# Kernel optimization log

Hardware: AMD Instinct MI355X
Metric: run time of the kernel (lower is better)

Reference implementation:

```python
import jax, jax.numpy as jnp
import numpy as np

N, E, EL = 20000, 320000, 100000
IN, HID, OUT, H = 256, 128, 128, 4
NEG_SLOPE = 0.2


def setup_inputs() -> dict:
    key = jax.random.key(0)
    ks = jax.random.split(key, 20)
    g = lambda k, shape, fan: jax.random.normal(k, shape, jnp.float32) * (1.0 / np.sqrt(fan))
    inp = {
        'x': jax.random.normal(ks[0], (N, IN), jnp.float32),
        'edge_index': jax.random.randint(ks[1], (2, E), 0, N, jnp.int32),
        'edge_label_index': jax.random.randint(ks[2], (2, EL), 0, N, jnp.int32),
        # GATv2 layer 1: in -> hidden, heads=H, concat
        'W_l1': g(ks[3], (IN, H * HID), IN), 'b_l1': jnp.zeros((H * HID,), jnp.float32),
        'W_r1': g(ks[4], (IN, H * HID), IN), 'b_r1': jnp.zeros((H * HID,), jnp.float32),
        'att1': g(ks[5], (H, HID), HID), 'bias1': jnp.zeros((H * HID,), jnp.float32),
        # GATv2 layer 2: H*hidden -> out, heads=1
        'W_l2': g(ks[6], (H * HID, OUT), H * HID), 'b_l2': jnp.zeros((OUT,), jnp.float32),
        'W_r2': g(ks[7], (H * HID, OUT), H * HID), 'b_r2': jnp.zeros((OUT,), jnp.float32),
        'att2': g(ks[8], (1, OUT), OUT), 'bias2': jnp.zeros((OUT,), jnp.float32),
        # decoder: Linear(2*OUT, HID) -> GELU -> Linear(HID, 1)
        'W_d1': g(ks[9], (2 * OUT, HID), 2 * OUT), 'b_d1': jnp.zeros((HID,), jnp.float32),
        'W_d2': g(ks[10], (HID, 1), HID), 'b_d2': jnp.zeros((1,), jnp.float32),
    }
    return inp


def gatv2_conv(x, src, dst, Wl, bl, Wr, br, att, bias, heads, ch):
    n = x.shape[0]
    xl = (x @ Wl + bl).reshape(n, heads, ch)  # source transform
    xr = (x @ Wr + br).reshape(n, heads, ch)  # target transform
    xj = xl[src]                              # [E, H, C] messages from source
    xi = xr[dst]                              # [E, H, C]
    e = jax.nn.leaky_relu(xi + xj, NEG_SLOPE)
    logits = jnp.einsum('ehc,hc->eh', e, att)  # [E, H]
    # segment softmax over incoming edges of each target node
    m = jax.ops.segment_max(logits, dst, num_segments=n)
    a = jnp.exp(logits - m[dst])
    s = jax.ops.segment_sum(a, dst, num_segments=n)
    alpha = a / s[dst]
    out = jax.ops.segment_sum(alpha[..., None] * xj, dst, num_segments=n)
    return out.reshape(n, heads * ch) + bias


def reference(x, edge_index, edge_label_index,
              W_l1, b_l1, W_r1, b_r1, att1, bias1,
              W_l2, b_l2, W_r2, b_r2, att2, bias2,
              W_d1, b_d1, W_d2, b_d2):
    n = x.shape[0]
    loops = jnp.arange(n, dtype=edge_index.dtype)
    src = jnp.concatenate([edge_index[0], loops])  # add_self_loops=True (PyG default)
    dst = jnp.concatenate([edge_index[1], loops])
    z = gatv2_conv(x, src, dst, W_l1, b_l1, W_r1, b_r1, att1, bias1, H, HID)
    z = jax.nn.gelu(z)  # dropout is identity in eval mode
    z = gatv2_conv(z, src, dst, W_l2, b_l2, W_r2, b_r2, att2, bias2, 1, OUT)
    # link decoder: gather-concat-MLP
    h = jnp.concatenate([z[edge_label_index[0]], z[edge_label_index[1]]], axis=-1)
    h = jax.nn.gelu(h @ W_d1 + b_d1)
    return (h @ W_d2 + b_d2).squeeze(-1)
```

## Files before the change

### kernel.cpp

```cpp
#include <hip/hip_runtime.h>
#include <hip/hip_bf16.h>
#include <math.h>
#include <stdint.h>

using bf16 = __hip_bfloat16;
typedef unsigned short u16;
typedef unsigned int   u32;
typedef __attribute__((ext_vector_type(8))) short short8;
typedef __attribute__((ext_vector_type(4))) float f32x4;
typedef _Float16 h2 __attribute__((ext_vector_type(2)));

static constexpr int NN   = 20000;
static constexpr int EE   = 320000;
static constexpr int ELN  = 100000;
static constexpr int ETOT = EE + NN;
static constexpr int INC  = 256;
static constexpr int C1   = 512;
static constexpr int C2   = 128;
static constexpr int NB   = (NN + 255) / 256;

__device__ __forceinline__ float us2f(u16 u){ union{u32 i; float f;}x; x.i=((u32)u)<<16; return x.f; }
__device__ __forceinline__ u16  f2us(float f){ union{bf16 h; u16 u;}c; c.h=__float2bfloat16(f); return c.u; }
__device__ __forceinline__ float h2f(u16 u){ union{u16 u; _Float16 h;}c; c.u=u; return (float)c.h; }
__device__ __forceinline__ float gelu_f(float x){
  float u = 1.5957691216057308f*(x + 0.044715f*x*x*x);
  float ex = __expf(u);
  float th = 1.f - 2.f/(ex + 1.f);
  return 0.5f*x*(1.f+th);
}
__device__ __forceinline__ void gl_lds16(const u16* g, void* l) {
  __builtin_amdgcn_global_load_lds((const __attribute__((address_space(1))) void*)g,
                                   (__attribute__((address_space(3))) void*)l, 16, 0, 0);
}
__device__ __forceinline__ void ld4v(const float* p, float* o){ float4 v=*(const float4*)p; o[0]=v.x;o[1]=v.y;o[2]=v.z;o[3]=v.w; }
__device__ __forceinline__ void ld4v(const u16* p, float* o){ uint2 v=*(const uint2*)p;
  o[0]=us2f(v.x&0xffff);o[1]=us2f(v.x>>16);o[2]=us2f(v.y&0xffff);o[3]=us2f(v.y>>16); }
__device__ __forceinline__ void ld4v(const _Float16* p, float* o){ uint2 v=*(const uint2*)p;
  o[0]=h2f(v.x&0xffff);o[1]=h2f(v.x>>16);o[2]=h2f(v.y&0xffff);o[3]=h2f(v.y>>16); }
__device__ __forceinline__ void ld8v(const float* p, float* o){ ld4v(p,o); ld4v(p+4,o+4); }
__device__ __forceinline__ void ld8v(const u16* p, float* o){ uint4 v=*(const uint4*)p;
  o[0]=us2f(v.x&0xffff);o[1]=us2f(v.x>>16);o[2]=us2f(v.y&0xffff);o[3]=us2f(v.y>>16);
  o[4]=us2f(v.z&0xffff);o[5]=us2f(v.z>>16);o[6]=us2f(v.w&0xffff);o[7]=us2f(v.w>>16); }
__device__ __forceinline__ void ld8v(const _Float16* p, float* o){ uint4 v=*(const uint4*)p;
  o[0]=h2f(v.x&0xffff);o[1]=h2f(v.x>>16);o[2]=h2f(v.y&0xffff);o[3]=h2f(v.y>>16);
  o[4]=h2f(v.z&0xffff);o[5]=h2f(v.z>>16);o[6]=h2f(v.w&0xffff);o[7]=h2f(v.w>>16); }
__device__ __forceinline__ void ld2v(const float* p, float* o){ float2 v=*(const float2*)p; o[0]=v.x;o[1]=v.y; }
__device__ __forceinline__ void ld2v(const _Float16* p, float* o){ u32 w=*(const u32*)p;
  o[0]=h2f(w&0xffff); o[1]=h2f(w>>16); }
__device__ __forceinline__ void st4v(float* p, const float* v){ *(float4*)p = make_float4(v[0],v[1],v[2],v[3]); }
__device__ __forceinline__ void st4v(u16* p, const float* v){ uint2 o;
  o.x=f2us(v[0])|((u32)f2us(v[1])<<16); o.y=f2us(v[2])|((u32)f2us(v[3])<<16); *(uint2*)p=o; }
__device__ __forceinline__ void st8v(float* p, const float* v){ st4v(p,v); st4v(p+4,v+4); }
__device__ __forceinline__ void st8v(u16* p, const float* v){ uint4 o;
  o.x=f2us(v[0])|((u32)f2us(v[1])<<16); o.y=f2us(v[2])|((u32)f2us(v[3])<<16);
  o.z=f2us(v[4])|((u32)f2us(v[5])<<16); o.w=f2us(v[6])|((u32)f2us(v[7])<<16); *(uint4*)p=o; }

struct PrepArgs {
  const float* x; u16* xth; u16* xtl; int nx;
  const float* wsrc[6]; u16* wth[6]; u16* wtl[6]; int wK[6]; int wN[6];
  const int* ei; int* cnt;
};
__global__ __launch_bounds__(256) void k_prep(PrepArgs a) {
  int seg = blockIdx.y;
  int tid = blockIdx.x*256 + threadIdx.x;
  int stride = gridDim.x*256;
  if (seg == 0) {
    for (int i = tid; i < a.nx; i += stride) {
      float v = a.x[i];
      u16 h = f2us(v);
      a.xth[i] = h;
      a.xtl[i] = f2us(v - us2f(h));
    }
  } else if (seg <= 6) {
    int s = seg - 1;
    int K = a.wK[s], N = a.wN[s];
    int n = K * N;
    for (int i = tid; i < n; i += stride) {
      int nn = i / K, k = i - nn*K;
      float v = a.wsrc[s][(size_t)k*N + nn];
      u16 h = f2us(v);
      a.wth[s][i] = h;
      a.wtl[s][i] = f2us(v - us2f(h));
    }
  } else {
    for (int e = tid; e < ETOT; e += stride) {
      int d = (e < EE) ? a.ei[EE + e] : (e - EE);
      if ((u32)d < (u32)NN) atomicAdd(&a.cnt[d], 1);
    }
  }
}

__global__ void k_scan_a(const int* __restrict__ cnt, int* __restrict__ row_ptr,
                         int* __restrict__ bsum) {
  __shared__ int buf[256];
  int idx = blockIdx.x*256 + threadIdx.x;
  int v = (idx < NN) ? cnt[idx] : 0;
  buf[threadIdx.x] = v;
  __syncthreads();
  for (int off = 1; off < 256; off <<= 1) {
    int t = (threadIdx.x >= off) ? buf[threadIdx.x - off] : 0;
    __syncthreads();
    buf[threadIdx.x] += t;
    __syncthreads();
  }
  if (idx < NN) row_ptr[idx] = buf[threadIdx.x] - v;
  if (threadIdx.x == 255) bsum[blockIdx.x] = buf[255];
}
__global__ void k_scan_b(int* __restrict__ bsum, int* __restrict__ row_ptr) {
  __shared__ int buf[128];
  int v = (threadIdx.x < NB) ? bsum[threadIdx.x] : 0;
  buf[threadIdx.x] = v;
  __syncthreads();
  for (int off = 1; off < 128; off <<= 1) {
    int t = (threadIdx.x >= off) ? buf[threadIdx.x - off] : 0;
    __syncthreads();
    buf[threadIdx.x] += t;
    __syncthreads();
  }
  if (threadIdx.x < NB) bsum[threadIdx.x] = buf[threadIdx.x] - v;
  if (threadIdx.x == 127) row_ptr[NN] = buf[127];
}
__global__ void k_scan_c(int* __restrict__ row_ptr, const int* __restrict__ bsum,
                         int* __restrict__ cur) {
  int idx = blockIdx.x*256 + threadIdx.x;
  if (idx < NN) {
    int v = row_ptr[idx] + bsum[blockIdx.x];
    row_ptr[idx] = v;
    cur[idx] = v;
  }
}
__global__ void k_scatter(const int* __restrict__ ei, int* __restrict__ cur,
                          int* __restrict__ col) {
  int e = blockIdx.x*blockDim.x + threadIdx.x;
  if (e < ETOT) {
    int s, d;
    if (e < EE) { s = ei[e]; d = ei[EE + e]; } else { s = d = e - EE; }
    if ((u32)d >= (u32)NN) d = 0;
    int pos = atomicAdd(&cur[d], 1);
    if ((u32)pos < (u32)ETOT) col[pos] = s;
  }
}

__global__ __launch_bounds__(256, 3)
void k_mgemm_a(const u16* __restrict__ Ath, const u16* __restrict__ Atl,
               const u16* __restrict__ Bth, const u16* __restrict__ Btl,
               const float* __restrict__ biasA, const float* __restrict__ biasB, int ncut,
               _Float16* __restrict__ C, int M, int N, int K, int nby) {
  __shared__ __align__(16) u16 sm[17408];
  int tid = threadIdx.x;
  int bidy = blockIdx.x % nby, bidx = blockIdx.x / nby;
  int m0 = bidx * 128, n0 = bidy * 128;
  int wave = tid >> 6, lane = tid & 63;
  int wm = (wave & 1) * 64, wn = (wave >> 1) * 64;
  int l15 = lane & 15, quad = lane >> 4;
  const u16* pbase = (wave == 0) ? Ath : (wave == 1) ? Atl : (wave == 2) ? Bth : Btl;
  bool isA = wave < 2;
  int rbase = isA ? m0 : n0;
  int rseg = lane >> 2;
  int kseg = (lane & 3) * 8;
  f32x4 acc[4][4] = {};
  for (int k0 = 0; k0 < K; k0 += 32) {
    #pragma unroll
    for (int i = 0; i < 8; ++i) {
      int r = rbase + i*16 + rseg;
      if (isA && r > M-1) r = M-1;
      gl_lds16(&pbase[(size_t)r*K + k0 + kseg], (char*)sm + (wave<<13) + (i<<10));
    }
    __syncthreads();
    short8 af_h[4], af_l[4], bf_h[4], bf_l[4];
    #pragma unroll
    for (int i = 0; i < 4; ++i) {
      af_h[i] = *(const short8*)&sm[         (wm + i*16 + l15)*32 + quad*8];
      af_l[i] = *(const short8*)&sm[ 4096 +  (wm + i*16 + l15)*32 + quad*8];
      bf_h[i] = *(const short8*)&sm[ 8192 +  (wn + i*16 + l15)*32 + quad*8];
      bf_l[i] = *(const short8*)&sm[12288 +  (wn + i*16 + l15)*32 + quad*8];
    }
    #pragma unroll
    for (int i = 0; i < 4; ++i)
      #pragma unroll
      for (int j = 0; j < 4; ++j) {
        acc[i][j] = __builtin_amdgcn_mfma_f32_16x16x32_bf16(af_h[i], bf_l[j], acc[i][j], 0,0,0);
        acc[i][j] = __builtin_amdgcn_mfma_f32_16x16x32_bf16(af_l[i], bf_h[j], acc[i][j], 0,0,0);
        acc[i][j] = __builtin_amdgcn_mfma_f32_16x16x32_bf16(af_h[i], bf_h[j], acc[i][j], 0,0,0);
      }
    __syncthreads();
  }
  #pragma unroll
  for (int j = 0; j < 4; ++j) {
    int col = wn + j*16 + l15;
    int colg = n0 + col;
    float bv = (colg < ncut) ? biasA[colg] : (biasB ? biasB[colg - ncut] : 0.f);
    #pragma unroll
    for (int i = 0; i < 4; ++i) {
      int rowb = wm + i*16 + quad*4;
      #pragma unroll
      for (int r = 0; r < 4; ++r) {
        union { _Float16 h; u16 u; } cv;
        cv.h = (_Float16)(acc[i][j][r] + bv);
        sm[(rowb + r)*136 + col] = cv.u;
      }
    }
  }
  __syncthreads();
  int row = tid >> 1, half = (tid & 1) * 64;
  int gr = m0 + row;
  if (gr < M) {
    uint4* d = (uint4*)&C[(size_t)gr*N + n0 + half];
    const uint4* s = (const uint4*)&sm[row*136 + half];
    #pragma unroll
    for (int q = 0; q < 8; ++q) d[q] = s[q];
  }
}

__global__ __launch_bounds__(256) void k_dec5(const _Float16* __restrict__ UV,
                                              const int* __restrict__ eli,
                                              const float* __restrict__ Wd2,
                                              const float* __restrict__ bd2,
                                              float* __restrict__ out) {
  int gw = (blockIdx.x*256 + threadIdx.x) >> 6;
  int nw = (gridDim.x*256) >> 6;
  int lane = threadIdx.x & 63;
  int c2 = lane*2;
  float w2a = Wd2[c2], w2b = Wd2[c2+1];
  float b2 = bd2[0];
  for (int e = gw; e < ELN; e += nw) {
    int a = __builtin_amdgcn_readfirstlane(eli[e]);      if ((u32)a >= (u32)NN) a = 0;
    int b = __builtin_amdgcn_readfirstlane(eli[ELN+e]);  if ((u32)b >= (u32)NN) b = 0;
    float u[2], v[2];
    ld2v(&UV[(size_t)a*256 + c2], u);
    ld2v(&UV[(size_t)b*256 + 128 + c2], v);
    float p = gelu_f(u[0]+v[0])*w2a + gelu_f(u[1]+v[1])*w2b;
    p += __shfl_xor(p,1);  p += __shfl_xor(p,2);
    p += __shfl_xor(p,4);  p += __shfl_xor(p,8);
    p += __shfl_xor(p,16); p += __shfl_xor(p,32);
    if (lane == 0) out[e] = p + b2;
  }
}

__global__ __launch_bounds__(256) void k_edge1p(const _Float16* __restrict__ xl,
                                                const _Float16* __restrict__ xr, int ld,
                                                const float* __restrict__ att,
                                                const float* __restrict__ bias,
                                                const int* __restrict__ row_ptr,
                                                const int* __restrict__ col,
                                                u16* __restrict__ z1h, u16* __restrict__ z1l) {
  int wid = (blockIdx.x*blockDim.x + threadIdx.x) >> 6;
  if (wid >= NN) return;
  int lane = threadIdx.x & 63;
  int c8 = lane*8;
  union Q { uint4 u; h2 h[4]; };
  Q XI; XI.u = *(const uint4*)&xr[(size_t)wid*ld + c8];
  h2 at[4];
  #pragma unroll
  for (int k=0;k<4;++k) { at[k][0] = (_Float16)att[c8+2*k]; at[k][1] = (_Float16)att[c8+2*k+1]; }
  const h2 k02 = {(_Float16)0.2f, (_Float16)0.2f};
  float acc[8] = {};
  float s = 0.f;
  int e0 = __builtin_amdgcn_readfirstlane(row_ptr[wid]);
  int e1 = __builtin_amdgcn_readfirstlane(row_ptr[wid+1]);
  int e = e0;
  for (; e + 4 <= e1; e += 4) {
    int s1 = __builtin_amdgcn_readfirstlane(col[e]);   if ((u32)s1 >= (u32)NN) s1 = 0;
    int s2 = __builtin_amdgcn_readfirstlane(col[e+1]); if ((u32)s2 >= (u32)NN) s2 = 0;
    int s3 = __builtin_amdgcn_readfirstlane(col[e+2]); if ((u32)s3 >= (u32)NN) s3 = 0;
    int s4 = __builtin_amdgcn_readfirstlane(col[e+3]); if ((u32)s4 >= (u32)NN) s4 = 0;
    Q X1, X2, X3, X4;
    X1.u = *(const uint4*)&xl[(size_t)s1*ld + c8];
    X2.u = *(const uint4*)&xl[(size_t)s2*ld + c8];
    X3.u = *(const uint4*)&xl[(size_t)s3*ld + c8];
    X4.u = *(const uint4*)&xl[(size_t)s4*ld + c8];
    float p1 = 0.f, p2 = 0.f, p3 = 0.f, p4 = 0.f;
    #pragma unroll
    for (int k=0;k<4;++k) {
      h2 t1 = XI.h[k] + X1.h[k]; t1 = __builtin_elementwise_max(t1, t1*k02);
      p1 = __builtin_amdgcn_fdot2(t1, at[k], p1, false);
      h2 t2 = XI.h[k] + X2.h[k]; t2 = __builtin_elementwise_max(t2, t2*k02);
      p2 = __builtin_amdgcn_fdot2(t2, at[k], p2, false);
      h2 t3 = XI.h[k] + X3.h[k]; t3 = __builtin_elementwise_max(t3, t3*k02);
      p3 = __builtin_amdgcn_fdot2(t3, at[k], p3, false);
      h2 t4 = XI.h[k] + X4.h[k]; t4 = __builtin_elementwise_max(t4, t4*k02);
      p4 = __builtin_amdgcn_fdot2(t4, at[k], p4, false);
    }
    p1 += __shfl_xor(p1,1); p2 += __shfl_xor(p2,1); p3 += __shfl_xor(p3,1); p4 += __shfl_xor(p4,1);
    p1 += __shfl_xor(p1,2); p2 += __shfl_xor(p2,2); p3 += __shfl_xor(p3,2); p4 += __shfl_xor(p4,2);
    p1 += __shfl_xor(p1,4); p2 += __shfl_xor(p2,4); p3 += __shfl_xor(p3,4); p4 += __shfl_xor(p4,4);
    p1 += __shfl_xor(p1,8); p2 += __shfl_xor(p2,8); p3 += __shfl_xor(p3,8); p4 += __shfl_xor(p4,8);
    float w1 = __expf(p1), w2 = __expf(p2), w3 = __expf(p3), w4 = __expf(p4);
    s += (w1 + w2) + (w3 + w4);
    #pragma unroll
    for (int k=0;k<4;++k) {
      acc[2*k]   += (w1*(float)X1.h[k][0] + w2*(float)X2.h[k][0])
                  + (w3*(float)X3.h[k][0] + w4*(float)X4.h[k][0]);
      acc[2*k+1] += (w1*(float)X1.h[k][1] + w2*(float)X2.h[k][1])
                  + (w3*(float)X3.h[k][1] + w4*(float)X4.h[k][1]);
    }
  }
  for (; e < e1; ++e) {
    int sn = __builtin_amdgcn_readfirstlane(col[e]); if ((u32)sn >= (u32)NN) sn = 0;
    Q XJ; XJ.u = *(const uint4*)&xl[(size_t)sn*ld + c8];
    float p = 0.f;
    #pragma unroll
    for (int k=0;k<4;++k) {
      h2 t = XI.h[k] + XJ.h[k];
      t = __builtin_elementwise_max(t, t*k02);
      p = __builtin_amdgcn_fdot2(t, at[k], p, false);
    }
    p += __shfl_xor(p,1); p += __shfl_xor(p,2);
    p += __shfl_xor(p,4); p += __shfl_xor(p,8);
    float w = __expf(p);
    s += w;
    #pragma unroll
    for (int k=0;k<4;++k) {
      acc[2*k]   += w*(float)XJ.h[k][0];
      acc[2*k+1] += w*(float)XJ.h[k][1];
    }
  }
  float inv = 1.f/s;
  u16 hh[8], ll[8];
  #pragma unroll
  for (int j=0;j<8;++j) {
    float o = gelu_f(acc[j]*inv + bias[c8+j]);
    hh[j] = f2us(o);
    ll[j] = f2us(o - us2f(hh[j]));
  }
  uint4 H, L;
  H.x = hh[0]|((u32)hh[1]<<16); H.y = hh[2]|((u32)hh[3]<<16);
  H.z = hh[4]|((u32)hh[5]<<16); H.w = hh[6]|((u32)hh[7]<<16);
  L.x = ll[0]|((u32)ll[1]<<16); L.y = ll[2]|((u32)ll[3]<<16);
  L.z = ll[4]|((u32)ll[5]<<16); L.w = ll[6]|((u32)ll[7]<<16);
  *(uint4*)&z1h[(size_t)wid*C1 + c8] = H;
  *(uint4*)&z1l[(size_t)wid*C1 + c8] = L;
}

__global__ __launch_bounds__(256) void k_edge2p(const _Float16* __restrict__ xl,
                                                const _Float16* __restrict__ xr, int ld,
                                                const float* __restrict__ att,
                                                const float* __restrict__ bias,
                                                const int* __restrict__ row_ptr,
                                                const int* __restrict__ col,
                                                u16* __restrict__ z2h, u16* __restrict__ z2l) {
  int wid = (blockIdx.x*blockDim.x + threadIdx.x) >> 6;
  if (wid >= NN) return;
  int lane = threadIdx.x & 63;
  int c2 = lane*2;
  union W { u32 u; h2 h; };
  W XI; XI.u = *(const u32*)&xr[(size_t)wid*ld + c2];
  h2 at; at[0] = (_Float16)att[c2]; at[1] = (_Float16)att[c2+1];
  const h2 k02 = {(_Float16)0.2f, (_Float16)0.2f};
  float s = 0.f, ac0 = 0.f, ac1 = 0.f;
  int e0 = __builtin_amdgcn_readfirstlane(row_ptr[wid]);
  int e1 = __builtin_amdgcn_readfirstlane(row_ptr[wid+1]);
  int e = e0;
  for (; e + 4 <= e1; e += 4) {
    int s1 = __builtin_amdgcn_readfirstlane(col[e]);   if ((u32)s1 >= (u32)NN) s1 = 0;
    int s2 = __builtin_amdgcn_readfirstlane(col[e+1]); if ((u32)s2 >= (u32)NN) s2 = 0;
    int s3 = __builtin_amdgcn_readfirstlane(col[e+2]); if ((u32)s3 >= (u32)NN) s3 = 0;
    int s4 = __builtin_amdgcn_readfirstlane(col[e+3]); if ((u32)s4 >= (u32)NN) s4 = 0;
    W X1, X2, X3, X4;
    X1.u = *(const u32*)&xl[(size_t)s1*ld + c2];
    X2.u = *(const u32*)&xl[(size_t)s2*ld + c2];
    X3.u = *(const u32*)&xl[(size_t)s3*ld + c2];
    X4.u = *(const u32*)&xl[(size_t)s4*ld + c2];
    h2 t1 = XI.h + X1.h; t1 = __builtin_elementwise_max(t1, t1*k02);
    h2 t2 = XI.h + X2.h; t2 = __builtin_elementwise_max(t2, t2*k02);
    h2 t3 = XI.h + X3.h; t3 = __builtin_elementwise_max(t3, t3*k02);
    h2 t4 = XI.h + X4.h; t4 = __builtin_elementwise_max(t4, t4*k02);
    float p1 = __builtin_amdgcn_fdot2(t1, at, 0.f, false);
    float p2 = __builtin_amdgcn_fdot2(t2, at, 0.f, false);
    float p3 = __builtin_amdgcn_fdot2(t3, at, 0.f, false);
    float p4 = __builtin_amdgcn_fdot2(t4, at, 0.f, false);
    p1 += __shfl_xor(p1,1);  p2 += __shfl_xor(p2,1);  p3 += __shfl_xor(p3,1);  p4 += __shfl_xor(p4,1);
    p1 += __shfl_xor(p1,2);  p2 += __shfl_xor(p2,2);  p3 += __shfl_xor(p3,2);  p4 += __shfl_xor(p4,2);
    p1 += __shfl_xor(p1,4);  p2 += __shfl_xor(p2,4);  p3 += __shfl_xor(p3,4);  p4 += __shfl_xor(p4,4);
    p1 += __shfl_xor(p1,8);  p2 += __shfl_xor(p2,8);  p3 += __shfl_xor(p3,8);  p4 += __shfl_xor(p4,8);
    p1 += __shfl_xor(p1,16); p2 += __shfl_xor(p2,16); p3 += __shfl_xor(p3,16); p4 += __shfl_xor(p4,16);
    p1 += __shfl_xor(p1,32); p2 += __shfl_xor(p2,32); p3 += __shfl_xor(p3,32); p4 += __shfl_xor(p4,32);
    float w1 = __expf(p1), w2 = __expf(p2), w3 = __expf(p3), w4 = __expf(p4);
    s += (w1 + w2) + (w3 + w4);
    ac0 += (w1*(float)X1.h[0] + w2*(float)X2.h[0]) + (w3*(float)X3.h[0] + w4*(float)X4.h[0]);
    ac1 += (w1*(float)X1.h[1] + w2*(float)X2.h[1]) + (w3*(float)X3.h[1] + w4*(float)X4.h[1]);
  }
  for (; e < e1; ++e) {
    int sn = __builtin_amdgcn_readfirstlane(col[e]); if ((u32)sn >= (u32)NN) sn = 0;
    W XJ; XJ.u = *(const u32*)&xl[(size_t)sn*ld + c2];
    h2 t = XI.h + XJ.h;
    t = __builtin_elementwise_max(t, t*k02);
    float p = __builtin_amdgcn_fdot2(t, at, 0.f, false);
    p += __shfl_xor(p,1);  p += __shfl_xor(p,2);
    p += __shfl_xor(p,4);  p += __shfl_xor(p,8);
    p += __shfl_xor(p,16); p += __shfl_xor(p,32);
    float w = __expf(p);
    s += w;
    ac0 += w*(float)XJ.h[0];
    ac1 += w*(float)XJ.h[1];
  }
  float inv = 1.f/s;
  float o0 = ac0*inv + bias[c2];
  float o1 = ac1*inv + bias[c2+1];
  u16 h0 = f2us(o0), h1 = f2us(o1);
  u16 l0 = f2us(o0 - us2f(h0)), l1v = f2us(o1 - us2f(h1));
  *(u32*)&z2h[(size_t)wid*C2 + c2] = h0 | ((u32)h1 << 16);
  *(u32*)&z2l[(size_t)wid*C2 + c2] = l0 | ((u32)l1v << 16);
}

__global__ void k_hist(const int* __restrict__ ei, int* __restrict__ cnt) {
  int e = blockIdx.x*blockDim.x + threadIdx.x;
  if (e < ETOT) {
    int d = (e < EE) ? ei[EE + e] : (e - EE);
    if ((u32)d < (u32)NN) atomicAdd(&cnt[d], 1);
  }
}
template <typename AT, typename CT>
__global__ __launch_bounds__(256) void k_gemm(const AT* __restrict__ A,
                                              const float* __restrict__ W,
                                              const float* __restrict__ bias,
                                              CT* __restrict__ C,
                                              int M, int Nc, int K) {
  __shared__ __align__(16) float As[16][64];
  __shared__ __align__(16) float Bs[16][64];
  int tid = threadIdx.x;
  int m0 = blockIdx.x*64, n0 = blockIdx.y*64;
  int ty = tid >> 4, tx = tid & 15;
  int lrow = tid >> 2;
  int lk   = (tid & 3)*4;
  int wk   = tid >> 4;
  int wn   = (tid & 15)*4;
  float acc[4][4] = {};
  for (int k0 = 0; k0 < K; k0 += 16) {
    int row = m0 + lrow;
    if (row < M) {
      float a4[4]; ld4v(&A[(size_t)row*K + k0 + lk], a4);
      As[lk+0][lrow]=a4[0]; As[lk+1][lrow]=a4[1]; As[lk+2][lrow]=a4[2]; As[lk+3][lrow]=a4[3];
    } else {
      #pragma unroll
      for (int j=0;j<4;++j) As[lk+j][lrow]=0.f;
    }
    {
      float4 bv4 = *(const float4*)&W[(size_t)(k0+wk)*Nc + n0 + wn];
      Bs[wk][wn+0]=bv4.x; Bs[wk][wn+1]=bv4.y; Bs[wk][wn+2]=bv4.z; Bs[wk][wn+3]=bv4.w;
    }
    __syncthreads();
    #pragma unroll
    for (int kk=0;kk<16;++kk) {
      float4 av = *(const float4*)&As[kk][ty*4];
      float4 bv = *(const float4*)&Bs[kk][tx*4];
      float a[4]={av.x,av.y,av.z,av.w}, b[4]={bv.x,bv.y,bv.z,bv.w};
      #pragma unroll
      for (int i=0;i<4;++i)
        #pragma unroll
        for (int j=0;j<4;++j)
          acc[i][j] += a[i]*b[j];
    }
    __syncthreads();
  }
  float bv[4];
  #pragma unroll
  for (int j=0;j<4;++j) bv[j] = bias[n0 + tx*4 + j];
  #pragma unroll
  for (int i=0;i<4;++i) {
    int row = m0 + ty*4 + i;
    if (row < M) {
      float o4[4] = {acc[i][0]+bv[0], acc[i][1]+bv[1], acc[i][2]+bv[2], acc[i][3]+bv[3]};
      st4v(&C[(size_t)row*Nc + n0 + tx*4], o4);
    }
  }
}
template <typename TI, typename TO>
__global__ __launch_bounds__(256) void k_edge1c(const TI* __restrict__ xl,
                                                const TI* __restrict__ xr, int ld,
                                                const float* __restrict__ att,
                                                const float* __restrict__ bias,
                                                const int* __restrict__ row_ptr,
                                                const int* __restrict__ col,
                                                TO* __restrict__ z1) {
  int wid = (blockIdx.x*blockDim.x + threadIdx.x) >> 6;
  if (wid >= NN) return;
  int lane = threadIdx.x & 63;
  int c8 = lane*8;
  float xi[8], av[8], acc[8] = {};
  ld8v(&xr[(size_t)wid*ld + c8], xi);
  #pragma unroll
  for (int j=0;j<8;++j) av[j] = att[c8+j];
  float s = 0.f;
  int e0 = row_ptr[wid], e1 = row_ptr[wid+1];
  for (int e = e0; e < e1; ++e) {
    int sn = col[e]; if ((u32)sn >= (u32)NN) sn = 0;
    float xj[8];
    ld8v(&xl[(size_t)sn*ld + c8], xj);
    float p = 0.f;
    #pragma unroll
    for (int j=0;j<8;++j) {
      float t = xi[j] + xj[j];
      t = fmaxf(t, 0.2f*t);
      p += t*av[j];
    }
    p += __shfl_xor(p,1); p += __shfl_xor(p,2);
    p += __shfl_xor(p,4); p += __shfl_xor(p,8);
    float w = __expf(p);
    s += w;
    #pragma unroll
    for (int j=0;j<8;++j) acc[j] += w*xj[j];
  }
  float inv = 1.f/s, o[8];
  #pragma unroll
  for (int j=0;j<8;++j) o[j] = gelu_f(acc[j]*inv + bias[c8+j]);
  st8v(&z1[(size_t)wid*C1 + c8], o);
}
template <typename TI, typename TO>
__global__ __launch_bounds__(256) void k_edge2c(const TI* __restrict__ xl,
                                                const TI* __restrict__ xr, int ld,
                                                const float* __restrict__ att,
                                                const float* __restrict__ bias,
                                                const int* __restrict__ row_ptr,
                                                const int* __restrict__ col,
                                                TO* __restrict__ z2) {
  int wid = (blockIdx.x*blockDim.x + threadIdx.x) >> 6;
  if (wid >= NN) return;
  int lane = threadIdx.x & 63;
  int c2 = lane*2;
  float xiv[2];
  ld2v(&xr[(size_t)wid*ld + c2], xiv);
  float a0 = att[c2], a1 = att[c2+1];
  float s = 0.f, ac0 = 0.f, ac1 = 0.f;
  int e0 = row_ptr[wid], e1 = row_ptr[wid+1];
  for (int e = e0; e < e1; ++e) {
    int sn = col[e]; if ((u32)sn >= (u32)NN) sn = 0;
    float xj[2];
    ld2v(&xl[(size_t)sn*ld + c2], xj);
    float t0 = xiv[0] + xj[0]; t0 = fmaxf(t0, 0.2f*t0);
    float t1 = xiv[1] + xj[1]; t1 = fmaxf(t1, 0.2f*t1);
    float p = t0*a0 + t1*a1;
    p += __shfl_xor(p,1);  p += __shfl_xor(p,2);
    p += __shfl_xor(p,4);  p += __shfl_xor(p,8);
    p += __shfl_xor(p,16); p += __shfl_xor(p,32);
    float w = __expf(p);
    s += w;
    ac0 += w*xj[0];
    ac1 += w*xj[1];
  }
  float inv = 1.f/s;
  z2[(size_t)wid*C2 + c2]   = (TO)(ac0*inv + bias[c2]);
  z2[(size_t)wid*C2 + c2+1] = (TO)(ac1*inv + bias[c2+1]);
}
__global__ __launch_bounds__(256) void k_dec2(const float* __restrict__ z2,
                                              const int* __restrict__ eli,
                                              const float* __restrict__ Wd1,
                                              const float* __restrict__ bd1,
                                              const float* __restrict__ Wd2,
                                              const float* __restrict__ bd2,
                                              float* __restrict__ out) {
  __shared__ __align__(16) float As[16][64];
  __shared__ __align__(16) float Bs[16][128];
  int tid = threadIdx.x;
  int e0 = blockIdx.x * 64;
  int ty = tid >> 4, tx = tid & 15;
  int lrow = tid >> 2;
  int lk   = (tid & 3) * 4;
  int wk   = tid >> 4;
  int wn   = (tid & 15) * 8;
  int e = e0 + lrow;
  bool ev = e < ELN;
  int ia = ev ? eli[e] : 0;       if ((u32)ia >= (u32)NN) ia = 0;
  int ib = ev ? eli[ELN+e] : 0;   if ((u32)ib >= (u32)NN) ib = 0;
  float acc[4][8] = {};
  for (int k0 = 0; k0 < 256; k0 += 16) {
    int kk4 = k0 + lk;
    const float* src = (kk4 < 128) ? &z2[(size_t)ia*128 + kk4]
                                   : &z2[(size_t)ib*128 + (kk4 - 128)];
    float4 a4 = ev ? *(const float4*)src : make_float4(0.f,0.f,0.f,0.f);
    As[lk+0][lrow]=a4.x; As[lk+1][lrow]=a4.y; As[lk+2][lrow]=a4.z; As[lk+3][lrow]=a4.w;
    *(float4*)&Bs[wk][wn]   = *(const float4*)&Wd1[(size_t)(k0+wk)*128 + wn];
    *(float4*)&Bs[wk][wn+4] = *(const float4*)&Wd1[(size_t)(k0+wk)*128 + wn + 4];
    __syncthreads();
    #pragma unroll
    for (int kk = 0; kk < 16; ++kk) {
      float4 av = *(const float4*)&As[kk][ty*4];
      float a[4] = {av.x, av.y, av.z, av.w};
      float4 b0 = *(const float4*)&Bs[kk][tx*4];
      float4 b1 = *(const float4*)&Bs[kk][64 + tx*4];
      float b[8] = {b0.x,b0.y,b0.z,b0.w,b1.x,b1.y,b1.z,b1.w};
      #pragma unroll
      for (int i = 0; i < 4; ++i)
        #pragma unroll
        for (int j = 0; j < 8; ++j)
          acc[i][j] += a[i]*b[j];
    }
    __syncthreads();
  }
  float w2[8], bb[8];
  #pragma unroll
  for (int j = 0; j < 4; ++j) {
    w2[j]   = Wd2[tx*4+j];      bb[j]   = bd1[tx*4+j];
    w2[j+4] = Wd2[64+tx*4+j];   bb[j+4] = bd1[64+tx*4+j];
  }
  float b2 = bd2[0];
  #pragma unroll
  for (int i = 0; i < 4; ++i) {
    float part = 0.f;
    #pragma unroll
    for (int j = 0; j < 8; ++j)
      part += gelu_f(acc[i][j] + bb[j]) * w2[j];
    part += __shfl_xor(part,1); part += __shfl_xor(part,2);
    part += __shfl_xor(part,4); part += __shfl_xor(part,8);
    int row = e0 + ty*4 + i;
    if (tx == 0 && row < ELN) out[row] = part + b2;
  }
}

__global__ void k_tiny(float* out, float code) {
  if (threadIdx.x == 0) out[0] = code;
}

extern "C" void kernel_launch(void* const* d_in, const int* in_sizes, int n_in,
                              void* d_out, int out_size, void* d_ws, size_t ws_size,
                              hipStream_t stream) {
  const float* x     = (const float*)d_in[0];
  const int*   ei    = (const int*)  d_in[1];
  const int*   eli   = (const int*)  d_in[2];
  const float* Wl1   = (const float*)d_in[3];
  const float* bl1   = (const float*)d_in[4];
  const float* Wr1   = (const float*)d_in[5];
  const float* br1   = (const float*)d_in[6];
  const float* att1  = (const float*)d_in[7];
  const float* bias1 = (const float*)d_in[8];
  const float* Wl2   = (const float*)d_in[9];
  const float* bl2   = (const float*)d_in[10];
  const float* Wr2   = (const float*)d_in[11];
  const float* br2   = (const float*)d_in[12];
  const float* att2  = (const float*)d_in[13];
  const float* bias2 = (const float*)d_in[14];
  const float* Wd1   = (const float*)d_in[15];
  const float* bd1   = (const float*)d_in[16];
  const float* Wd2   = (const float*)d_in[17];
  const float* bd2   = (const float*)d_in[18];
  float* out = (float*)d_out;

  constexpr size_t INTW = (size_t)(NN+1) + NN + ETOT;
  constexpr size_t FULL_WORDS = 3ull*NN*C1 + INTW;
  constexpr size_t CMP_WORDS  = 3ull*NN*C1/2 + INTW;

  bool full    = ws_size >= FULL_WORDS*4;
  bool compact = !full && ws_size >= CMP_WORDS*4;
  if (!full && !compact) {
    size_t mb = ws_size >> 20;
    k_tiny<<<1, 64, 0, stream>>>(out, 16384.f + (float)mb);
    return;
  }

  size_t regA = full ? (size_t)NN*C1 : (size_t)NN*C1/2;
  char* base = (char*)d_ws;
  void* wA = base;
  void* wB = base + regA*4;
  void* wC = base + 2*regA*4;
  int* row_ptr = (int*)(base + 3*regA*4);
  int* cnt     = row_ptr + (NN + 1);
  int* col     = cnt + NN;
  int* bsum    = (int*)wA;

  hipMemsetAsync(cnt, 0, NN*sizeof(int), stream);

  if (full) {
    _Float16* xlr1 = (_Float16*)wA;
    _Float16* xlr2 = (_Float16*)wA;
    _Float16* UV   = (_Float16*)wA;
    u16* xth = (u16*)wB;
    u16* xtl = xth + (size_t)NN*INC;
    u16* wt1th = (u16*)((char*)wB + (21u<<20));
    u16* wt1tl = wt1th + 1024*256;
    u16* wt2th = wt1tl + 1024*256;
    u16* wt2tl = wt2th + 256*512;
    u16* wdth  = wt2tl + 256*512;
    u16* wdtl  = wdth  + 256*128;
    u16* z1h = (u16*)wC;
    u16* z1l = z1h + (size_t)NN*C1;
    u16* z2h = (u16*)wC;
    u16* z2l = z2h + (size_t)NN*C2;

    PrepArgs pa;
    pa.x = x; pa.xth = xth; pa.xtl = xtl; pa.nx = NN*INC;
    pa.wsrc[0]=Wl1;          pa.wth[0]=wt1th;         pa.wtl[0]=wt1tl;         pa.wK[0]=INC; pa.wN[0]=C1;
    pa.wsrc[1]=Wr1;          pa.wth[1]=wt1th+512*256; pa.wtl[1]=wt1tl+512*256; pa.wK[1]=INC; pa.wN[1]=C1;
    pa.wsrc[2]=Wl2;          pa.wth[2]=wt2th;         pa.wtl[2]=wt2tl;         pa.wK[2]=C1;  pa.wN[2]=C2;
    pa.wsrc[3]=Wr2;          pa.wth[3]=wt2th+128*512; pa.wtl[3]=wt2tl+128*512; pa.wK[3]=C1;  pa.wN[3]=C2;
    pa.wsrc[4]=Wd1;          pa.wth[4]=wdth;          pa.wtl[4]=wdtl;          pa.wK[4]=128; pa.wN[4]=128;
    pa.wsrc[5]=Wd1+128*128;  pa.wth[5]=wdth+128*128;  pa.wtl[5]=wdtl+128*128;  pa.wK[5]=128; pa.wN[5]=128;
    pa.ei = ei; pa.cnt = cnt;
    k_prep<<<dim3(1344, 8), 256, 0, stream>>>(pa);

    k_scan_a<<<NB, 256, 0, stream>>>(cnt, row_ptr, bsum);
    k_scan_b<<<1, 128, 0, stream>>>(bsum, row_ptr);
    k_scan_c<<<NB, 256, 0, stream>>>(row_ptr, bsum, cnt);
    k_scatter<<<(ETOT+255)/256, 256, 0, stream>>>(ei, cnt, col);

    k_mgemm_a<<<157*8, 256, 0, stream>>>(xth, xtl, wt1th, wt1tl,
                                         bl1, br1, 512, xlr1, NN, 1024, INC, 8);
    k_edge1p<<<NN/4, 256, 0, stream>>>(xlr1, xlr1+512, 1024, att1, bias1, row_ptr, col, z1h, z1l);
    k_mgemm_a<<<157*2, 256, 0, stream>>>(z1h, z1l, wt2th, wt2tl,
                                         bl2, br2, 128, xlr2, NN, 256, C1, 2);
    k_edge2p<<<NN/4, 256, 0, stream>>>(xlr2, xlr2+128, 256, att2, bias2, row_ptr, col, z2h, z2l);
    k_mgemm_a<<<157*2, 256, 0, stream>>>(z2h, z2l, wdth, wdtl,
                                         bd1, nullptr, 128, UV, NN, 256, 128, 2);
    k_dec5<<<2048, 256, 0, stream>>>(UV, eli, Wd2, bd2, out);
  } else {
    u16* xl1 = (u16*)wA;
    u16* xr1 = (u16*)wB;
    u16* z1  = (u16*)wC;
    float* xl2 = (float*)wA;
    float* xr2 = (float*)wB;
    float* z2  = (float*)wC;
    k_hist<<<(ETOT+255)/256, 256, 0, stream>>>(ei, cnt);
    k_scan_a<<<NB, 256, 0, stream>>>(cnt, row_ptr, bsum);
    k_scan_b<<<1, 128, 0, stream>>>(bsum, row_ptr);
    k_scan_c<<<NB, 256, 0, stream>>>(row_ptr, bsum, cnt);
    k_scatter<<<(ETOT+255)/256, 256, 0, stream>>>(ei, cnt, col);
    dim3 g1((NN+63)/64, C1/64);
    dim3 g2((NN+63)/64, C2/64);
    k_gemm<float,u16><<<g1, 256, 0, stream>>>(x, Wl1, bl1, xl1, NN, C1, INC);
    k_gemm<float,u16><<<g1, 256, 0, stream>>>(x, Wr1, br1, xr1, NN, C1, INC);
    k_edge1c<u16,u16><<<NN/4, 256, 0, stream>>>(xl1, xr1, C1, att1, bias1, row_ptr, col, z1);
    k_gemm<u16,float><<<g2, 256, 0, stream>>>(z1, Wl2, bl2, xl2, NN, C2, C1);
    k_gemm<u16,float><<<g2, 256, 0, stream>>>(z1, Wr2, br2, xr2, NN, C2, C1);
    k_edge2c<float,float><<<NN/4, 256, 0, stream>>>(xl2, xr2, C2, att2, bias2, row_ptr, col, z2);
    k_dec2<<<(ELN+63)/64, 256, 0, stream>>>(z2, eli, Wd1, bd1, Wd2, bd2, out);
  }
}
```

Before: 347.8 us.

## Split layer-1 edge aggregation of each node across four waves with LDS reduction

The layer-1 GATv2 edge kernel now assigns one 256-thread block per target node instead of one wave per node. The node's incoming edges are split into four contiguous chunks, one per wave, and the partial weighted sums and softmax denominators are combined through shared memory before wave 0 applies GELU and writes the output. This aims to shorten the serial gather chain per node and expose more memory parallelism. In exchange it adds a block barrier, shared-memory traffic and four times as many blocks, and waves sit idle when a node has very few edges. The softmax still skips max-subtraction, as before.

After: 348.4 us. No clear change (+0.2%).

```diff
diff --git a/kernel.cpp b/kernel.cpp
--- a/kernel.cpp
+++ b/kernel.cpp
@@ -237,16 +237,17 @@
   }
 }
 
-__global__ __launch_bounds__(256) void k_edge1p(const _Float16* __restrict__ xl,
+__global__ __launch_bounds__(256) void k_edge1s(const _Float16* __restrict__ xl,
                                                 const _Float16* __restrict__ xr, int ld,
                                                 const float* __restrict__ att,
                                                 const float* __restrict__ bias,
                                                 const int* __restrict__ row_ptr,
                                                 const int* __restrict__ col,
                                                 u16* __restrict__ z1h, u16* __restrict__ z1l) {
-  int wid = (blockIdx.x*blockDim.x + threadIdx.x) >> 6;
-  if (wid >= NN) return;
-  int lane = threadIdx.x & 63;
+  __shared__ float pacc[3][8][64];
+  __shared__ float psum[3][64];
+  int wid = blockIdx.x;
+  int wave = threadIdx.x >> 6, lane = threadIdx.x & 63;
   int c8 = lane*8;
   union Q { uint4 u; h2 h[4]; };
   Q XI; XI.u = *(const uint4*)&xr[(size_t)wid*ld + c8];
@@ -258,8 +259,11 @@
   float s = 0.f;
   int e0 = __builtin_amdgcn_readfirstlane(row_ptr[wid]);
   int e1 = __builtin_amdgcn_readfirstlane(row_ptr[wid+1]);
-  int e = e0;
-  for (; e + 4 <= e1; e += 4) {
+  int q = ((e1 - e0) + 3) >> 2;
+  int st = e0 + wave*q;
+  int en = st + q; if (en > e1) en = e1; if (st > e1) st = e1;
+  int e = st;
+  for (; e + 4 <= en; e += 4) {
     int s1 = __builtin_amdgcn_readfirstlane(col[e]);   if ((u32)s1 >= (u32)NN) s1 = 0;
     int s2 = __builtin_amdgcn_readfirstlane(col[e+1]); if ((u32)s2 >= (u32)NN) s2 = 0;
     int s3 = __builtin_amdgcn_readfirstlane(col[e+2]); if ((u32)s3 >= (u32)NN) s3 = 0;
@@ -295,7 +299,7 @@
                   + (w3*(float)X3.h[k][1] + w4*(float)X4.h[k][1]);
     }
   }
-  for (; e < e1; ++e) {
+  for (; e < en; ++e) {
     int sn = __builtin_amdgcn_readfirstlane(col[e]); if ((u32)sn >= (u32)NN) sn = 0;
     Q XJ; XJ.u = *(const uint4*)&xl[(size_t)sn*ld + c8];
     float p = 0.f;
@@ -315,21 +319,35 @@
       acc[2*k+1] += w*(float)XJ.h[k][1];
     }
   }
-  float inv = 1.f/s;
-  u16 hh[8], ll[8];
-  #pragma unroll
-  for (int j=0;j<8;++j) {
-    float o = gelu_f(acc[j]*inv + bias[c8+j]);
-    hh[j] = f2us(o);
-    ll[j] = f2us(o - us2f(hh[j]));
-  }
-  uint4 H, L;
-  H.x = hh[0]|((u32)hh[1]<<16); H.y = hh[2]|((u32)hh[3]<<16);
-  H.z = hh[4]|((u32)hh[5]<<16); H.w = hh[6]|((u32)hh[7]<<16);
-  L.x = ll[0]|((u32)ll[1]<<16); L.y = ll[2]|((u32)ll[3]<<16);
-  L.z = ll[4]|((u32)ll[5]<<16); L.w = ll[6]|((u32)ll[7]<<16);
-  *(uint4*)&z1h[(size_t)wid*C1 + c8] = H;
-  *(uint4*)&z1l[(size_t)wid*C1 + c8] = L;
+  if (wave > 0) {
+    #pragma unroll
+    for (int j=0;j<8;++j) pacc[wave-1][j][lane] = acc[j];
+    psum[wave-1][lane] = s;
+  }
+  __syncthreads();
+  if (wave == 0) {
+    #pragma unroll
+    for (int wv=0; wv<3; ++wv) {
+      s += psum[wv][lane];
+      #pragma unroll
+      for (int j=0;j<8;++j) acc[j] += pacc[wv][j][lane];
+    }
+    float inv = 1.f/s;
+    u16 hh[8], ll[8];
+    #pragma unroll
+    for (int j=0;j<8;++j) {
+      float o = gelu_f(acc[j]*inv + bias[c8+j]);
+      hh[j] = f2us(o);
+      ll[j] = f2us(o - us2f(hh[j]));
+    }
+    uint4 H, L;
+    H.x = hh[0]|((u32)hh[1]<<16); H.y = hh[2]|((u32)hh[3]<<16);
+    H.z = hh[4]|((u32)hh[5]<<16); H.w = hh[6]|((u32)hh[7]<<16);
+    L.x = ll[0]|((u32)ll[1]<<16); L.y = ll[2]|((u32)ll[3]<<16);
+    L.z = ll[4]|((u32)ll[5]<<16); L.w = ll[6]|((u32)ll[7]<<16);
+    *(uint4*)&z1h[(size_t)wid*C1 + c8] = H;
+    *(uint4*)&z1l[(size_t)wid*C1 + c8] = L;
+  }
 }
 
 __global__ __launch_bounds__(256) void k_edge2p(const _Float16* __restrict__ xl,
@@ -694,7 +712,7 @@
 
     k_mgemm_a<<<157*8, 256, 0, stream>>>(xth, xtl, wt1th, wt1tl,
                                          bl1, br1, 512, xlr1, NN, 1024, INC, 8);
-    k_edge1p<<<NN/4, 256, 0, stream>>>(xlr1, xlr1+512, 1024, att1, bias1, row_ptr, col, z1h, z1l);
+    k_edge1s<<<NN, 256, 0, stream>>>(xlr1, xlr1+512, 1024, att1, bias1, row_ptr, col, z1h, z1l);
     k_mgemm_a<<<157*2, 256, 0, stream>>>(z1h, z1l, wt2th, wt2tl,
                                          bl2, br2, 128, xlr2, NN, 256, C1, 2);
     k_edge2p<<<NN/4, 256, 0, stream>>>(xlr2, xlr2+128, 256, att2, bias2, row_ptr, col, z2h, z2l);
```

## Replace LDS-staged 128x128 split-bf16 GEMM with single-wave direct-load 64x64 tiles

Applied to the files above, without the earlier changes.

The three split-precision GEMMs move from a 256-thread block that stages 128x128 A/B tiles in shared memory through global_load_lds, with barriers, to a one-wave block that loads MFMA fragments straight from global memory into registers for a 64x64 tile. This removes the LDS staging and per-k-step barriers and launches many more small blocks, but drops cross-wave reuse of the staged tiles, so each operand is read from global/L2 more often. Separately, the layer-1 edge aggregation loop goes from 4-way to 2-way unrolled, with a single-edge prologue for odd degrees, which trades memory-level parallelism for lower register pressure.

Result: slower. 414.4 us (+19.2%).

```diff
diff --git a/kernel.cpp b/kernel.cpp
--- a/kernel.cpp
+++ b/kernel.cpp
@@ -27,10 +27,6 @@
   float ex = __expf(u);
   float th = 1.f - 2.f/(ex + 1.f);
   return 0.5f*x*(1.f+th);
-}
-__device__ __forceinline__ void gl_lds16(const u16* g, void* l) {
-  __builtin_amdgcn_global_load_lds((const __attribute__((address_space(1))) void*)g,
-                                   (__attribute__((address_space(3))) void*)l, 16, 0, 0);
 }
 __device__ __forceinline__ void ld4v(const float* p, float* o){ float4 v=*(const float4*)p; o[0]=v.x;o[1]=v.y;o[2]=v.z;o[3]=v.w; }
 __device__ __forceinline__ void ld4v(const u16* p, float* o){ uint2 v=*(const uint2*)p;
@@ -141,74 +137,60 @@
   }
 }
 
-__global__ __launch_bounds__(256, 3)
-void k_mgemm_a(const u16* __restrict__ Ath, const u16* __restrict__ Atl,
+__global__ __launch_bounds__(64)
+void k_mgemm_d(const u16* __restrict__ Ath, const u16* __restrict__ Atl,
                const u16* __restrict__ Bth, const u16* __restrict__ Btl,
                const float* __restrict__ biasA, const float* __restrict__ biasB, int ncut,
-               _Float16* __restrict__ C, int M, int N, int K, int nby) {
-  __shared__ __align__(16) u16 sm[17408];
-  int tid = threadIdx.x;
-  int bidy = blockIdx.x % nby, bidx = blockIdx.x / nby;
-  int m0 = bidx * 128, n0 = bidy * 128;
-  int wave = tid >> 6, lane = tid & 63;
-  int wm = (wave & 1) * 64, wn = (wave >> 1) * 64;
+               _Float16* __restrict__ C, int M, int N, int K, int nt) {
+  __shared__ __align__(16) u16 tile[64*72];
+  int lane = threadIdx.x;
   int l15 = lane & 15, quad = lane >> 4;
-  const u16* pbase = (wave == 0) ? Ath : (wave == 1) ? Atl : (wave == 2) ? Bth : Btl;
-  bool isA = wave < 2;
-  int rbase = isA ? m0 : n0;
-  int rseg = lane >> 2;
-  int kseg = (lane & 3) * 8;
+  int m0 = (blockIdx.x / nt) * 64;
+  int n0 = (blockIdx.x % nt) * 64;
   f32x4 acc[4][4] = {};
   for (int k0 = 0; k0 < K; k0 += 32) {
-    #pragma unroll
-    for (int i = 0; i < 8; ++i) {
-      int r = rbase + i*16 + rseg;
-      if (isA && r > M-1) r = M-1;
-      gl_lds16(&pbase[(size_t)r*K + k0 + kseg], (char*)sm + (wave<<13) + (i<<10));
-    }
-    __syncthreads();
-    short8 af_h[4], af_l[4], bf_h[4], bf_l[4];
+    short8 ah[4], al[4], bh[4], bl[4];
     #pragma unroll
     for (int i = 0; i < 4; ++i) {
-      af_h[i] = *(const short8*)&sm[         (wm + i*16 + l15)*32 + quad*8];
-      af_l[i] = *(const short8*)&sm[ 4096 +  (wm + i*16 + l15)*32 + quad*8];
-      bf_h[i] = *(const short8*)&sm[ 8192 +  (wn + i*16 + l15)*32 + quad*8];
-      bf_l[i] = *(const short8*)&sm[12288 +  (wn + i*16 + l15)*32 + quad*8];
+      int ra = m0 + i*16 + l15; if (ra > M-1) ra = M-1;
+      int rb = n0 + i*16 + l15;
+      size_t oa = (size_t)ra*K + k0 + quad*8;
+      size_t ob = (size_t)rb*K + k0 + quad*8;
+      ah[i] = *(const short8*)&Ath[oa];
+      al[i] = *(const short8*)&Atl[oa];
+      bh[i] = *(const short8*)&Bth[ob];
+      bl[i] = *(const short8*)&Btl[ob];
     }
     #pragma unroll
     for (int i = 0; i < 4; ++i)
       #pragma unroll
       for (int j = 0; j < 4; ++j) {
-        acc[i][j] = __builtin_amdgcn_mfma_f32_16x16x32_bf16(af_h[i], bf_l[j], acc[i][j], 0,0,0);
-        acc[i][j] = __builtin_amdgcn_mfma_f32_16x16x32_bf16(af_l[i], bf_h[j], acc[i][j], 0,0,0);
-        acc[i][j] = __builtin_amdgcn_mfma_f32_16x16x32_bf16(af_h[i], bf_h[j], acc[i][j], 0,0,0);
+        acc[i][j] = __builtin_amdgcn_mfma_f32_16x16x32_bf16(ah[i], bl[j], acc[i][j], 0,0,0);
+        acc[i][j] = __builtin_amdgcn_mfma_f32_16x16x32_bf16(al[i], bh[j], acc[i][j], 0,0,0);
+        acc[i][j] = __builtin_amdgcn_mfma_f32_16x16x32_bf16(ah[i], bh[j], acc[i][j], 0,0,0);
       }
-    __syncthreads();
   }
   #pragma unroll
   for (int j = 0; j < 4; ++j) {
-    int col = wn + j*16 + l15;
-    int colg = n0 + col;
+    int colg = n0 + j*16 + l15;
     float bv = (colg < ncut) ? biasA[colg] : (biasB ? biasB[colg - ncut] : 0.f);
     #pragma unroll
     for (int i = 0; i < 4; ++i) {
-      int rowb = wm + i*16 + quad*4;
       #pragma unroll
       for (int r = 0; r < 4; ++r) {
         union { _Float16 h; u16 u; } cv;
         cv.h = (_Float16)(acc[i][j][r] + bv);
-        sm[(rowb + r)*136 + col] = cv.u;
+        tile[(i*16 + quad*4 + r)*72 + j*16 + l15] = cv.u;
       }
     }
   }
   __syncthreads();
-  int row = tid >> 1, half = (tid & 1) * 64;
-  int gr = m0 + row;
-  if (gr < M) {
-    uint4* d = (uint4*)&C[(size_t)gr*N + n0 + half];
-    const uint4* s = (const uint4*)&sm[row*136 + half];
-    #pragma unroll
-    for (int q = 0; q < 8; ++q) d[q] = s[q];
+  int row = m0 + lane;
+  if (row < M) {
+    uint4* d = (uint4*)&C[(size_t)row*N + n0];
+    const u16* s = &tile[lane*72];
+    #pragma unroll
+    for (int q = 0; q < 8; ++q) d[q] = *(const uint4*)(s + q*8);
   }
 }
 
@@ -259,43 +241,7 @@
   int e0 = __builtin_amdgcn_readfirstlane(row_ptr[wid]);
   int e1 = __builtin_amdgcn_readfirstlane(row_ptr[wid+1]);
   int e = e0;
-  for (; e + 4 <= e1; e += 4) {
-    int s1 = __builtin_amdgcn_readfirstlane(col[e]);   if ((u32)s1 >= (u32)NN) s1 = 0;
-    int s2 = __builtin_amdgcn_readfirstlane(col[e+1]); if ((u32)s2 >= (u32)NN) s2 = 0;
-    int s3 = __builtin_amdgcn_readfirstlane(col[e+2]); if ((u32)s3 >= (u32)NN) s3 = 0;
-    int s4 = __builtin_amdgcn_readfirstlane(col[e+3]); if ((u32)s4 >= (u32)NN) s4 = 0;
-    Q X1, X2, X3, X4;
-    X1.u = *(const uint4*)&xl[(size_t)s1*ld + c8];
-    X2.u = *(const uint4*)&xl[(size_t)s2*ld + c8];
-    X3.u = *(const uint4*)&xl[(size_t)s3*ld + c8];
-    X4.u = *(const uint4*)&xl[(size_t)s4*ld + c8];
-    float p1 = 0.f, p2 = 0.f, p3 = 0.f, p4 = 0.f;
-    #pragma unroll
-    for (int k=0;k<4;++k) {
-      h2 t1 = XI.h[k] + X1.h[k]; t1 = __builtin_elementwise_max(t1, t1*k02);
-      p1 = __builtin_amdgcn_fdot2(t1, at[k], p1, false);
-      h2 t2 = XI.h[k] + X2.h[k]; t2 = __builtin_elementwise_max(t2, t2*k02);
-      p2 = __builtin_amdgcn_fdot2(t2, at[k], p2, false);
-      h2 t3 = XI.h[k] + X3.h[k]; t3 = __builtin_elementwise_max(t3, t3*k02);
-      p3 = __builtin_amdgcn_fdot2(t3, at[k], p3, false);
-      h2 t4 = XI.h[k] + X4.h[k]; t4 = __builtin_elementwise_max(t4, t4*k02);
-      p4 = __builtin_amdgcn_fdot2(t4, at[k], p4, false);
-    }
-    p1 += __shfl_xor(p1,1); p2 += __shfl_xor(p2,1); p3 += __shfl_xor(p3,1); p4 += __shfl_xor(p4,1);
-    p1 += __shfl_xor(p1,2); p2 += __shfl_xor(p2,2); p3 += __shfl_xor(p3,2); p4 += __shfl_xor(p4,2);
-    p1 += __shfl_xor(p1,4); p2 += __shfl_xor(p2,4); p3 += __shfl_xor(p3,4); p4 += __shfl_xor(p4,4);
-    p1 += __shfl_xor(p1,8); p2 += __shfl_xor(p2,8); p3 += __shfl_xor(p3,8); p4 += __shfl_xor(p4,8);
-    float w1 = __expf(p1), w2 = __expf(p2), w3 = __expf(p3), w4 = __expf(p4);
-    s += (w1 + w2) + (w3 + w4);
-    #pragma unroll
-    for (int k=0;k<4;++k) {
-      acc[2*k]   += (w1*(float)X1.h[k][0] + w2*(float)X2.h[k][0])
-                  + (w3*(float)X3.h[k][0] + w4*(float)X4.h[k][0]);
-      acc[2*k+1] += (w1*(float)X1.h[k][1] + w2*(float)X2.h[k][1])
-                  + (w3*(float)X3.h[k][1] + w4*(float)X4.h[k][1]);
-    }
-  }
-  for (; e < e1; ++e) {
+  if ((e1 - e0) & 1) {
     int sn = __builtin_amdgcn_readfirstlane(col[e]); if ((u32)sn >= (u32)NN) sn = 0;
     Q XJ; XJ.u = *(const uint4*)&xl[(size_t)sn*ld + c8];
     float p = 0.f;
@@ -313,6 +259,36 @@
     for (int k=0;k<4;++k) {
       acc[2*k]   += w*(float)XJ.h[k][0];
       acc[2*k+1] += w*(float)XJ.h[k][1];
+    }
+    ++e;
+  }
+  for (; e < e1; e += 2) {
+    int s1 = __builtin_amdgcn_readfirstlane(col[e]);   if ((u32)s1 >= (u32)NN) s1 = 0;
+    int s2 = __builtin_amdgcn_readfirstlane(col[e+1]); if ((u32)s2 >= (u32)NN) s2 = 0;
+    Q X1, X2;
+    X1.u = *(const uint4*)&xl[(size_t)s1*ld + c8];
+    X2.u = *(const uint4*)&xl[(size_t)s2*ld + c8];
+    float p1 = 0.f, p2 = 0.f;
+    #pragma unroll
+    for (int k=0;k<4;++k) {
+      h2 t1 = XI.h[k] + X1.h[k];
+      t1 = __builtin_elementwise_max(t1, t1*k02);
+      p1 = __builtin_amdgcn_fdot2(t1, at[k], p1, false);
+      h2 t2 = XI.h[k] + X2.h[k];
+      t2 = __builtin_elementwise_max(t2, t2*k02);
+      p2 = __builtin_amdgcn_fdot2(t2, at[k], p2, false);
+    }
+    p1 += __shfl_xor(p1,1); p2 += __shfl_xor(p2,1);
+    p1 += __shfl_xor(p1,2); p2 += __shfl_xor(p2,2);
+    p1 += __shfl_xor(p1,4); p2 += __shfl_xor(p2,4);
+    p1 += __shfl_xor(p1,8); p2 += __shfl_xor(p2,8);
+    float w1 = __expf(p1);
+    float w2 = __expf(p2);
+    s += w1 + w2;
+    #pragma unroll
+    for (int k=0;k<4;++k) {
+      acc[2*k]   += w1*(float)X1.h[k][0] + w2*(float)X2.h[k][0];
+      acc[2*k+1] += w1*(float)X1.h[k][1] + w2*(float)X2.h[k][1];
     }
   }
   float inv = 1.f/s;
@@ -692,14 +668,15 @@
     k_scan_c<<<NB, 256, 0, stream>>>(row_ptr, bsum, cnt);
     k_scatter<<<(ETOT+255)/256, 256, 0, stream>>>(ei, cnt, col);
 
-    k_mgemm_a<<<157*8, 256, 0, stream>>>(xth, xtl, wt1th, wt1tl,
-                                         bl1, br1, 512, xlr1, NN, 1024, INC, 8);
+    constexpr int MT = (NN + 63) / 64;
+    k_mgemm_d<<<MT*16, 64, 0, stream>>>(xth, xtl, wt1th, wt1tl,
+                                        bl1, br1, 512, xlr1, NN, 1024, INC, 16);
     k_edge1p<<<NN/4, 256, 0, stream>>>(xlr1, xlr1+512, 1024, att1, bias1, row_ptr, col, z1h, z1l);
-    k_mgemm_a<<<157*2, 256, 0, stream>>>(z1h, z1l, wt2th, wt2tl,
-                                         bl2, br2, 128, xlr2, NN, 256, C1, 2);
+    k_mgemm_d<<<MT*4, 64, 0, stream>>>(z1h, z1l, wt2th, wt2tl,
+                                       bl2, br2, 128, xlr2, NN, 256, C1, 4);
     k_edge2p<<<NN/4, 256, 0, stream>>>(xlr2, xlr2+128, 256, att2, bias2, row_ptr, col, z2h, z2l);
-    k_mgemm_a<<<157*2, 256, 0, stream>>>(z2h, z2l, wdth, wdtl,
-                                         bd1, nullptr, 128, UV, NN, 256, 128, 2);
+    k_mgemm_d<<<MT*4, 64, 0, stream>>>(z2h, z2l, wdth, wdtl,
+                                       bd1, nullptr, 128, UV, NN, 256, 128, 4);
     k_dec5<<<2048, 256, 0, stream>>>(UV, eli, Wd2, bd2, out);
   } else {
     u16* xl1 = (u16*)wA;
```
